# Performance work log

Measured on AMD Instinct MI355X. Metric: run time of the kernel, lower is better.

## Reference

```python
import jax, jax.numpy as jnp
import numpy as np

B, T = 64, 512
N_EMB, HIDDEN, VOCAB = 768, 256, 3072


def setup_inputs() -> dict:
    key = jax.random.key(0)
    ks = jax.random.split(key, 5)
    def xavier(k, shape):
        bound = float(np.sqrt(6.0 / (shape[0] + shape[1])))
        return jax.random.uniform(k, shape, jnp.float32, -bound, bound)
    return {
        "idx": jax.random.randint(ks[0], (B, T), 0, VOCAB),
        "emb_table": jax.random.normal(ks[1], (VOCAB, N_EMB), jnp.float32),
        "Wxh": xavier(ks[2], (N_EMB, HIDDEN)),
        "Whh": xavier(ks[3], (HIDDEN, HIDDEN)),
        "Wy": xavier(ks[4], (HIDDEN, VOCAB)),
        "By": jnp.zeros((VOCAB,), jnp.float32),
        "Bh": jnp.zeros((HIDDEN,), jnp.float32),
    }


def reference(idx, emb_table, Wxh, Whh, Wy, By, Bh):
    # embedded: [B, T, E] -> scan over time with hidden carry [B, H]
    embedded = emb_table[idx]                      # gather
    xWxh = jnp.einsum('bte,eh->tbh', embedded, Wxh)  # precompute input projection

    def step(hidden, x_t):
        hidden = jnp.tanh(x_t + hidden @ Whh + Bh)
        return hidden, None

    h0 = jnp.zeros((idx.shape[0], Whh.shape[0]), embedded.dtype)
    hidden, _ = jax.lax.scan(step, h0, xWxh)
    # return_sequences=False: only the last step's output is returned
    out = hidden @ Wy + By
    return out, hidden
```

## Files before the change

kernel.cpp:

```cpp
#include <hip/hip_runtime.h>
#include <hip/hip_bf16.h>

typedef _Float16 half8 __attribute__((ext_vector_type(8)));
typedef float f32x4 __attribute__((ext_vector_type(4)));

#define B_SZ 64
#define T_SZ 512
#define E_SZ 768
#define H_SZ 256
#define V_SZ 3072

#define WS_X     0u
#define WS_WT    16777216u
#define WS_WF    17170432u
#define WS_H     17301504u

static __device__ __forceinline__ float fast_tanh(float x) {
  float e = __builtin_amdgcn_exp2f(x * 2.8853900817779268f);
  return 1.0f - 2.0f * __builtin_amdgcn_rcpf(1.0f + e);
}

__global__ __launch_bounds__(256) void k0_convert(
    const float* __restrict__ Wxh,
    const float* __restrict__ Whh,
    _Float16* __restrict__ Wt,
    _Float16* __restrict__ Wf)
{
  int gid = blockIdx.x * 256 + threadIdx.x;
  if (gid < E_SZ * H_SZ) {
    int e = gid >> 8, h = gid & 255;
    Wt[h * E_SZ + e] = (_Float16)Wxh[gid];
  }
  if (gid < 65536) {
    int j = gid & 7, lane = (gid >> 3) & 63, kt = (gid >> 9) & 7, nt = gid >> 12;
    int quad = lane >> 4, n16 = lane & 15;
    int row = kt * 32 + quad * 8 + j, col = nt * 16 + n16;
    Wf[gid] = (_Float16)Whh[row * H_SZ + col];
  }
}

__global__ __launch_bounds__(256) void k1_xproj(
    const int* __restrict__ idx,
    const float* __restrict__ emb,
    const _Float16* __restrict__ Wt,
    _Float16* __restrict__ x)
{
  const int tid  = threadIdx.x;
  const int w    = tid >> 6;
  const int lane = tid & 63;
  const int m16  = lane & 15;
  const int quad = lane >> 4;
  const int r = blockIdx.x * 64 + w * 16 + m16;
  const int t = r >> 6;
  const int b = r & 63;
  const int erow = idx[b * T_SZ + t];
  const float* Arow = emb + (size_t)erow * E_SZ + quad * 8;

  __shared__ __align__(16) _Float16 bp[16 * 64 * 8];
  int n_[4], kb_[4];
#pragma unroll
  for (int pp = 0; pp < 4; ++pp) {
    int f = tid + 256 * pp;
    n_[pp]  = ((f >> 6) << 4) | (f & 15);
    kb_[pp] = (f >> 4) & 3;
  }
  uint4 stg[4];
#pragma unroll
  for (int pp = 0; pp < 4; ++pp)
    stg[pp] = *(const uint4*)(Wt + (size_t)n_[pp] * E_SZ + kb_[pp] * 8);
  f32x4 af0 = *(const f32x4*)(Arow);
  f32x4 af1 = *(const f32x4*)(Arow + 4);

  f32x4 acc[16];
#pragma unroll
  for (int n = 0; n < 16; ++n) { f32x4 z = {0.f, 0.f, 0.f, 0.f}; acc[n] = z; }

#pragma unroll 1
  for (int ki = 0; ki < 24; ++ki) {
    __syncthreads();
#pragma unroll
    for (int pp = 0; pp < 4; ++pp)
      *(uint4*)(bp + (size_t)(tid + 256 * pp) * 8) = stg[pp];
    __syncthreads();
    if (ki < 23) {
#pragma unroll
      for (int pp = 0; pp < 4; ++pp)
        stg[pp] = *(const uint4*)(Wt + (size_t)n_[pp] * E_SZ + (ki + 1) * 32 + kb_[pp] * 8);
    }
    f32x4 af0n = af0, af1n = af1;
    if (ki < 23) {
      af0n = *(const f32x4*)(Arow + (ki + 1) * 32);
      af1n = *(const f32x4*)(Arow + (ki + 1) * 32 + 4);
    }
    half8 a;
#pragma unroll
    for (int e = 0; e < 4; ++e) { a[e] = (_Float16)af0[e]; a[4 + e] = (_Float16)af1[e]; }
#pragma unroll
    for (int nt = 0; nt < 16; ++nt) {
      half8 bb = *(const half8*)(bp + (size_t)(nt * 64 + lane) * 8);
      acc[nt] = __builtin_amdgcn_mfma_f32_16x16x32_f16(a, bb, acc[nt], 0, 0, 0);
    }
    af0 = af0n; af1 = af1n;
  }
  const int rbase = blockIdx.x * 64 + w * 16 + quad * 4;
#pragma unroll
  for (int nt = 0; nt < 16; ++nt) {
    const int col = nt * 16 + m16;
#pragma unroll
    for (int rg = 0; rg < 4; ++rg) {
      x[(size_t)(rbase + rg) * H_SZ + col] = (_Float16)acc[nt][rg];
    }
  }
}

#define LDFRAG(C, KT, R0, R1, R2, R3) { \
  uint4 q = Wf4[(((size_t)(w * 4 + C) * 8 + KT) * 64) + lane]; \
  asm volatile("v_accvgpr_write_b32 a" #R0 ", %0" :: "v"(q.x) : "a" #R0); \
  asm volatile("v_accvgpr_write_b32 a" #R1 ", %0" :: "v"(q.y) : "a" #R1); \
  asm volatile("v_accvgpr_write_b32 a" #R2 ", %0" :: "v"(q.z) : "a" #R2); \
  asm volatile("v_accvgpr_write_b32 a" #R3 ", %0" :: "v"(q.w) : "a" #R3); }

__global__ __launch_bounds__(256) void k2_rnn(
    const _Float16* __restrict__ Wf,
    const _Float16* __restrict__ x,
    const float* __restrict__ Bh,
    float* __restrict__ hout,
    float* __restrict__ hidout)
{
  const int b    = blockIdx.x;
  const int tid  = threadIdx.x;
  const int w    = tid >> 6;
  const int lane = tid & 63;
  const int quad = lane >> 4;
  __shared__ __align__(16) _Float16 hb[2][H_SZ];
  const uint4* Wf4 = (const uint4*)Wf;

  LDFRAG(0,0,  0,  1,  2,  3)  LDFRAG(0,1,  4,  5,  6,  7)
  LDFRAG(0,2,  8,  9, 10, 11)  LDFRAG(0,3, 12, 13, 14, 15)
  LDFRAG(0,4, 16, 17, 18, 19)  LDFRAG(0,5, 20, 21, 22, 23)
  LDFRAG(0,6, 24, 25, 26, 27)  LDFRAG(0,7, 28, 29, 30, 31)
  LDFRAG(1,0, 32, 33, 34, 35)  LDFRAG(1,1, 36, 37, 38, 39)
  LDFRAG(1,2, 40, 41, 42, 43)  LDFRAG(1,3, 44, 45, 46, 47)
  LDFRAG(1,4, 48, 49, 50, 51)  LDFRAG(1,5, 52, 53, 54, 55)
  LDFRAG(1,6, 56, 57, 58, 59)  LDFRAG(1,7, 60, 61, 62, 63)
  LDFRAG(2,0, 64, 65, 66, 67)  LDFRAG(2,1, 68, 69, 70, 71)
  LDFRAG(2,2, 72, 73, 74, 75)  LDFRAG(2,3, 76, 77, 78, 79)
  LDFRAG(2,4, 80, 81, 82, 83)  LDFRAG(2,5, 84, 85, 86, 87)
  LDFRAG(2,6, 88, 89, 90, 91)  LDFRAG(2,7, 92, 93, 94, 95)
  LDFRAG(3,0, 96, 97, 98, 99)  LDFRAG(3,1,100,101,102,103)
  LDFRAG(3,2,104,105,106,107)  LDFRAG(3,3,108,109,110,111)
  LDFRAG(3,4,112,113,114,115)  LDFRAG(3,5,116,117,118,119)
  LDFRAG(3,6,120,121,122,123)  LDFRAG(3,7,124,125,126,127)

  const float bhj = Bh[tid];
  const _Float16* xp = x + b * H_SZ + tid;
  _Float16 xq = xp[0];
  f32x4 zero4 = {0.f, 0.f, 0.f, 0.f};
  asm volatile("" : "+v"(zero4));
  hb[1][tid] = (_Float16)0.f;
  float hval = 0.f;
  __syncthreads();

#pragma unroll 1
  for (int t = 0; t < T_SZ; ++t) {
    const int tn = (t < T_SZ - 1) ? (t + 1) : t;
    _Float16 xn = xp[(size_t)tn * (B_SZ * H_SZ)];
    const _Float16* hr = hb[(t + 1) & 1];
    half8 va0 = *(const half8*)(hr +   0 + quad * 8);
    half8 va1 = *(const half8*)(hr +  32 + quad * 8);
    half8 va2 = *(const half8*)(hr +  64 + quad * 8);
    half8 va3 = *(const half8*)(hr +  96 + quad * 8);
    half8 va4 = *(const half8*)(hr + 128 + quad * 8);
    half8 va5 = *(const half8*)(hr + 160 + quad * 8);
    half8 va6 = *(const half8*)(hr + 192 + quad * 8);
    half8 va7 = *(const half8*)(hr + 224 + quad * 8);
    f32x4 acc0, acc1, acc2, acc3;
    asm volatile(
      "v_mfma_f32_16x16x32_f16 %[t0], %[a0], a[0:3], %[z]\n\t"
      "v_mfma_f32_16x16x32_f16 %[t1], %[a0], a[32:35], %[z]\n\t"
      "v_mfma_f32_16x16x32_f16 %[t2], %[a0], a[64:67], %[z]\n\t"
      "v_mfma_f32_16x16x32_f16 %[t3], %[a0], a[96:99], %[z]\n\t"
      "v_mfma_f32_16x16x32_f16 %[t0], %[a1], a[4:7], %[t0]\n\t"
      "v_mfma_f32_16x16x32_f16 %[t1], %[a1], a[36:39], %[t1]\n\t"
      "v_mfma_f32_16x16x32_f16 %[t2], %[a1], a[68:71], %[t2]\n\t"
      "v_mfma_f32_16x16x32_f16 %[t3], %[a1], a[100:103], %[t3]\n\t"
      "v_mfma_f32_16x16x32_f16 %[t0], %[a2], a[8:11], %[t0]\n\t"
      "v_mfma_f32_16x16x32_f16 %[t1], %[a2], a[40:43], %[t1]\n\t"
      "v_mfma_f32_16x16x32_f16 %[t2], %[a2], a[72:75], %[t2]\n\t"
      "v_mfma_f32_16x16x32_f16 %[t3], %[a2], a[104:107], %[t3]\n\t"
      "v_mfma_f32_16x16x32_f16 %[t0], %[a3], a[12:15], %[t0]\n\t"
      "v_mfma_f32_16x16x32_f16 %[t1], %[a3], a[44:47], %[t1]\n\t"
      "v_mfma_f32_16x16x32_f16 %[t2], %[a3], a[76:79], %[t2]\n\t"
      "v_mfma_f32_16x16x32_f16 %[t3], %[a3], a[108:111], %[t3]\n\t"
      "v_mfma_f32_16x16x32_f16 %[t0], %[a4], a[16:19], %[t0]\n\t"
      "v_mfma_f32_16x16x32_f16 %[t1], %[a4], a[48:51], %[t1]\n\t"
      "v_mfma_f32_16x16x32_f16 %[t2], %[a4], a[80:83], %[t2]\n\t"
      "v_mfma_f32_16x16x32_f16 %[t3], %[a4], a[112:115], %[t3]\n\t"
      "v_mfma_f32_16x16x32_f16 %[t0], %[a5], a[20:23], %[t0]\n\t"
      "v_mfma_f32_16x16x32_f16 %[t1], %[a5], a[52:55], %[t1]\n\t"
      "v_mfma_f32_16x16x32_f16 %[t2], %[a5], a[84:87], %[t2]\n\t"
      "v_mfma_f32_16x16x32_f16 %[t3], %[a5], a[116:119], %[t3]\n\t"
      "v_mfma_f32_16x16x32_f16 %[t0], %[a6], a[24:27], %[t0]\n\t"
      "v_mfma_f32_16x16x32_f16 %[t1], %[a6], a[56:59], %[t1]\n\t"
      "v_mfma_f32_16x16x32_f16 %[t2], %[a6], a[88:91], %[t2]\n\t"
      "v_mfma_f32_16x16x32_f16 %[t3], %[a6], a[120:123], %[t3]\n\t"
      "v_mfma_f32_16x16x32_f16 %[t0], %[a7], a[28:31], %[t0]\n\t"
      "v_mfma_f32_16x16x32_f16 %[t1], %[a7], a[60:63], %[t1]\n\t"
      "v_mfma_f32_16x16x32_f16 %[t2], %[a7], a[92:95], %[t2]\n\t"
      "v_mfma_f32_16x16x32_f16 %[t3], %[a7], a[124:127], %[t3]\n\t"
      "s_nop 7\n\t"
      "s_nop 7"
      : [t0] "=&v"(acc0), [t1] "=&v"(acc1), [t2] "=&v"(acc2), [t3] "=&v"(acc3)
      : [a0] "v"(va0), [a1] "v"(va1), [a2] "v"(va2), [a3] "v"(va3),
        [a4] "v"(va4), [a5] "v"(va5), [a6] "v"(va6), [a7] "v"(va7),
        [z] "v"(zero4));
    float v0 = acc0[0], v1 = acc1[0], v2 = acc2[0], v3 = acc3[0];
    float ylo = (quad & 1) ? v1 : v0;
    float yhi = (quad & 1) ? v3 : v2;
    float y   = (quad & 2) ? yhi : ylo;
    hval = fast_tanh(y + (float)xq + bhj);
    hb[t & 1][tid] = (_Float16)hval;
    __syncthreads();
    xq = xn;
  }
  hout[b * H_SZ + tid] = hval;
  hidout[b * H_SZ + tid] = hval;
}

__global__ __launch_bounds__(256) void k3_out(
    const float* __restrict__ h,
    const float* __restrict__ Wy,
    const float* __restrict__ By,
    float* __restrict__ out)
{
  __shared__ float hs[H_SZ];
  const int c = blockIdx.x;
  const int b = blockIdx.y;
  const int v = c * 256 + threadIdx.x;
  hs[threadIdx.x] = h[b * H_SZ + threadIdx.x];
  __syncthreads();
  float acc = By[v];
#pragma unroll 8
  for (int jj = 0; jj < H_SZ; ++jj) {
    acc += hs[jj] * Wy[(size_t)jj * V_SZ + v];
  }
  out[(size_t)b * V_SZ + v] = acc;
}

extern "C" void kernel_launch(void* const* d_in, const int* in_sizes, int n_in,
                              void* d_out, int out_size, void* d_ws, size_t ws_size,
                              hipStream_t stream)
{
  const int*   idx = (const int*)d_in[0];
  const float* emb = (const float*)d_in[1];
  const float* Wxh = (const float*)d_in[2];
  const float* Whh = (const float*)d_in[3];
  const float* Wy  = (const float*)d_in[4];
  const float* By  = (const float*)d_in[5];
  const float* Bh  = (const float*)d_in[6];

  char* ws = (char*)d_ws;
  _Float16* x    = (_Float16*)(ws + WS_X);
  _Float16* Wt   = (_Float16*)(ws + WS_WT);
  _Float16* Wf   = (_Float16*)(ws + WS_WF);
  float*    hbuf = (float*)(ws + WS_H);

  float* out    = (float*)d_out;
  float* hidout = out + (size_t)B_SZ * V_SZ;

  k0_convert<<<768, 256, 0, stream>>>(Wxh, Whh, Wt, Wf);
  k1_xproj  <<<512, 256, 0, stream>>>(idx, emb, Wt, x);
  k2_rnn    <<<64, 256, 0, stream>>>(Wf, x, Bh, hbuf, hidout);
  k3_out    <<<dim3(12, 64), 256, 0, stream>>>(hbuf, Wy, By, out);
}
```

Before: 403.0 us.

## Double-buffer LDS weight tiles in xproj and split RNN MFMA asm per k-step

The input-projection kernel now keeps two LDS buffers for the weight tile, so the next tile is written while the current one is consumed. This cuts the two barriers per iteration down to one. The recurrent kernel's single 32-MFMA inline-asm block is split into eight smaller asm statements, one per k-slice, which lets the compiler schedule the LDS loads of later hidden fragments between MFMA groups. The cost is double the LDS in k1, and the split asm loses the guarantee of ordering and hazard padding between MFMAs, which now depends on asm volatile ordering.

Result: faster. 386.3 us (-4.2%).

```diff
diff --git a/kernel.cpp b/kernel.cpp
--- a/kernel.cpp
+++ b/kernel.cpp
@@ -56,7 +56,7 @@
   const int erow = idx[b * T_SZ + t];
   const float* Arow = emb + (size_t)erow * E_SZ + quad * 8;
 
-  __shared__ __align__(16) _Float16 bp[16 * 64 * 8];
+  __shared__ __align__(16) _Float16 bp[2][16 * 64 * 8];
   int n_[4], kb_[4];
 #pragma unroll
   for (int pp = 0; pp < 4; ++pp) {
@@ -75,20 +75,19 @@
 #pragma unroll
   for (int n = 0; n < 16; ++n) { f32x4 z = {0.f, 0.f, 0.f, 0.f}; acc[n] = z; }
 
+#pragma unroll
+  for (int pp = 0; pp < 4; ++pp)
+    *(uint4*)(bp[0] + (size_t)(tid + 256 * pp) * 8) = stg[pp];
+  __syncthreads();
+
 #pragma unroll 1
   for (int ki = 0; ki < 24; ++ki) {
-    __syncthreads();
-#pragma unroll
-    for (int pp = 0; pp < 4; ++pp)
-      *(uint4*)(bp + (size_t)(tid + 256 * pp) * 8) = stg[pp];
-    __syncthreads();
+    const _Float16* cur = bp[ki & 1];
+    f32x4 af0n = af0, af1n = af1;
     if (ki < 23) {
 #pragma unroll
       for (int pp = 0; pp < 4; ++pp)
         stg[pp] = *(const uint4*)(Wt + (size_t)n_[pp] * E_SZ + (ki + 1) * 32 + kb_[pp] * 8);
-    }
-    f32x4 af0n = af0, af1n = af1;
-    if (ki < 23) {
       af0n = *(const f32x4*)(Arow + (ki + 1) * 32);
       af1n = *(const f32x4*)(Arow + (ki + 1) * 32 + 4);
     }
@@ -97,8 +96,14 @@
     for (int e = 0; e < 4; ++e) { a[e] = (_Float16)af0[e]; a[4 + e] = (_Float16)af1[e]; }
 #pragma unroll
     for (int nt = 0; nt < 16; ++nt) {
-      half8 bb = *(const half8*)(bp + (size_t)(nt * 64 + lane) * 8);
+      half8 bb = *(const half8*)(cur + (size_t)(nt * 64 + lane) * 8);
       acc[nt] = __builtin_amdgcn_mfma_f32_16x16x32_f16(a, bb, acc[nt], 0, 0, 0);
+    }
+    if (ki < 23) {
+#pragma unroll
+      for (int pp = 0; pp < 4; ++pp)
+        *(uint4*)(bp[(ki + 1) & 1] + (size_t)(tid + 256 * pp) * 8) = stg[pp];
+      __syncthreads();
     }
     af0 = af0n; af1 = af1n;
   }
@@ -119,6 +124,35 @@
   asm volatile("v_accvgpr_write_b32 a" #R1 ", %0" :: "v"(q.y) : "a" #R1); \
   asm volatile("v_accvgpr_write_b32 a" #R2 ", %0" :: "v"(q.z) : "a" #R2); \
   asm volatile("v_accvgpr_write_b32 a" #R3 ", %0" :: "v"(q.w) : "a" #R3); }
+
+#define MFMA_K0(A0, Z) \
+  asm volatile( \
+    "v_mfma_f32_16x16x32_f16 %[t0], %[a], a[0:3],   %[z]\n\t" \
+    "v_mfma_f32_16x16x32_f16 %[t1], %[a], a[32:35], %[z]\n\t" \
+    "v_mfma_f32_16x16x32_f16 %[t2], %[a], a[64:67], %[z]\n\t" \
+    "v_mfma_f32_16x16x32_f16 %[t3], %[a], a[96:99], %[z]" \
+    : [t0] "=&v"(acc0), [t1] "=&v"(acc1), [t2] "=&v"(acc2), [t3] "=&v"(acc3) \
+    : [a] "v"(A0), [z] "v"(Z));
+
+#define MFMA_KT(A0, B0, B1, B2, B3) \
+  asm volatile( \
+    "v_mfma_f32_16x16x32_f16 %[t0], %[a], a[" #B0 "], %[t0]\n\t" \
+    "v_mfma_f32_16x16x32_f16 %[t1], %[a], a[" #B1 "], %[t1]\n\t" \
+    "v_mfma_f32_16x16x32_f16 %[t2], %[a], a[" #B2 "], %[t2]\n\t" \
+    "v_mfma_f32_16x16x32_f16 %[t3], %[a], a[" #B3 "], %[t3]" \
+    : [t0] "+v"(acc0), [t1] "+v"(acc1), [t2] "+v"(acc2), [t3] "+v"(acc3) \
+    : [a] "v"(A0));
+
+#define MFMA_K7(A0, B0, B1, B2, B3) \
+  asm volatile( \
+    "v_mfma_f32_16x16x32_f16 %[t0], %[a], a[" #B0 "], %[t0]\n\t" \
+    "v_mfma_f32_16x16x32_f16 %[t1], %[a], a[" #B1 "], %[t1]\n\t" \
+    "v_mfma_f32_16x16x32_f16 %[t2], %[a], a[" #B2 "], %[t2]\n\t" \
+    "v_mfma_f32_16x16x32_f16 %[t3], %[a], a[" #B3 "], %[t3]\n\t" \
+    "s_nop 7\n\t" \
+    "s_nop 7" \
+    : [t0] "+v"(acc0), [t1] "+v"(acc1), [t2] "+v"(acc2), [t3] "+v"(acc3) \
+    : [a] "v"(A0));
 
 __global__ __launch_bounds__(256) void k2_rnn(
     const _Float16* __restrict__ Wf,
@@ -175,45 +209,14 @@
     half8 va6 = *(const half8*)(hr + 192 + quad * 8);
     half8 va7 = *(const half8*)(hr + 224 + quad * 8);
     f32x4 acc0, acc1, acc2, acc3;
-    asm volatile(
-      "v_mfma_f32_16x16x32_f16 %[t0], %[a0], a[0:3], %[z]\n\t"
-      "v_mfma_f32_16x16x32_f16 %[t1], %[a0], a[32:35], %[z]\n\t"
-      "v_mfma_f32_16x16x32_f16 %[t2], %[a0], a[64:67], %[z]\n\t"
-      "v_mfma_f32_16x16x32_f16 %[t3], %[a0], a[96:99], %[z]\n\t"
-      "v_mfma_f32_16x16x32_f16 %[t0], %[a1], a[4:7], %[t0]\n\t"
-      "v_mfma_f32_16x16x32_f16 %[t1], %[a1], a[36:39], %[t1]\n\t"
-      "v_mfma_f32_16x16x32_f16 %[t2], %[a1], a[68:71], %[t2]\n\t"
-      "v_mfma_f32_16x16x32_f16 %[t3], %[a1], a[100:103], %[t3]\n\t"
-      "v_mfma_f32_16x16x32_f16 %[t0], %[a2], a[8:11], %[t0]\n\t"
-      "v_mfma_f32_16x16x32_f16 %[t1], %[a2], a[40:43], %[t1]\n\t"
-      "v_mfma_f32_16x16x32_f16 %[t2], %[a2], a[72:75], %[t2]\n\t"
-      "v_mfma_f32_16x16x32_f16 %[t3], %[a2], a[104:107], %[t3]\n\t"
-      "v_mfma_f32_16x16x32_f16 %[t0], %[a3], a[12:15], %[t0]\n\t"
-      "v_mfma_f32_16x16x32_f16 %[t1], %[a3], a[44:47], %[t1]\n\t"
-      "v_mfma_f32_16x16x32_f16 %[t2], %[a3], a[76:79], %[t2]\n\t"
-      "v_mfma_f32_16x16x32_f16 %[t3], %[a3], a[108:111], %[t3]\n\t"
-      "v_mfma_f32_16x16x32_f16 %[t0], %[a4], a[16:19], %[t0]\n\t"
-      "v_mfma_f32_16x16x32_f16 %[t1], %[a4], a[48:51], %[t1]\n\t"
-      "v_mfma_f32_16x16x32_f16 %[t2], %[a4], a[80:83], %[t2]\n\t"
-      "v_mfma_f32_16x16x32_f16 %[t3], %[a4], a[112:115], %[t3]\n\t"
-      "v_mfma_f32_16x16x32_f16 %[t0], %[a5], a[20:23], %[t0]\n\t"
-      "v_mfma_f32_16x16x32_f16 %[t1], %[a5], a[52:55], %[t1]\n\t"
-      "v_mfma_f32_16x16x32_f16 %[t2], %[a5], a[84:87], %[t2]\n\t"
-      "v_mfma_f32_16x16x32_f16 %[t3], %[a5], a[116:119], %[t3]\n\t"
-      "v_mfma_f32_16x16x32_f16 %[t0], %[a6], a[24:27], %[t0]\n\t"
-      "v_mfma_f32_16x16x32_f16 %[t1], %[a6], a[56:59], %[t1]\n\t"
-      "v_mfma_f32_16x16x32_f16 %[t2], %[a6], a[88:91], %[t2]\n\t"
-      "v_mfma_f32_16x16x32_f16 %[t3], %[a6], a[120:123], %[t3]\n\t"
-      "v_mfma_f32_16x16x32_f16 %[t0], %[a7], a[28:31], %[t0]\n\t"
-      "v_mfma_f32_16x16x32_f16 %[t1], %[a7], a[60:63], %[t1]\n\t"
-      "v_mfma_f32_16x16x32_f16 %[t2], %[a7], a[92:95], %[t2]\n\t"
-      "v_mfma_f32_16x16x32_f16 %[t3], %[a7], a[124:127], %[t3]\n\t"
-      "s_nop 7\n\t"
-      "s_nop 7"
-      : [t0] "=&v"(acc0), [t1] "=&v"(acc1), [t2] "=&v"(acc2), [t3] "=&v"(acc3)
-      : [a0] "v"(va0), [a1] "v"(va1), [a2] "v"(va2), [a3] "v"(va3),
-        [a4] "v"(va4), [a5] "v"(va5), [a6] "v"(va6), [a7] "v"(va7),
-        [z] "v"(zero4));
+    MFMA_K0(va0, zero4)
+    MFMA_KT(va1,   4:7,  36:39,  68:71, 100:103)
+    MFMA_KT(va2,  8:11,  40:43,  72:75, 104:107)
+    MFMA_KT(va3, 12:15,  44:47,  76:79, 108:111)
+    MFMA_KT(va4, 16:19,  48:51,  80:83, 112:115)
+    MFMA_KT(va5, 20:23,  52:55,  84:87, 116:119)
+    MFMA_KT(va6, 24:27,  56:59,  88:91, 120:123)
+    MFMA_K7(va7, 28:31,  60:63,  92:95, 124:127)
     float v0 = acc0[0], v1 = acc1[0], v2 = acc2[0], v3 = acc3[0];
     float ylo = (quad & 1) ? v1 : v0;
     float yhi = (quad & 1) ? v3 : v2;
```
